# Optimization experiments

Hardware: AMD Instinct MI355X
Metric: run time of the kernel (lower is better)

The kernel has to match this reference:

```python
import jax, jax.numpy as jnp
import numpy as np

NEG_SLOPE = 0.2
EPS = 1e-6
K = 16


def vec_lna(x, Wf, Wd):
    # x: (B, Cin, 3, ...). Vector-neuron linear + VN-LeakyReLU.
    p = jnp.einsum('oc,bc...->bo...', Wf, x)          # features (B, Cout, 3, ...)
    d = jnp.einsum('oc,bc...->bo...', Wd, x)          # directions (B, Cd, 3, ...), Cd=Cout or 1 (shared)
    dot = jnp.sum(p * d, axis=2, keepdims=True)
    dsq = jnp.sum(d * d, axis=2, keepdims=True)
    p_ref = p - (dot / (dsq + EPS)) * d               # reflect negative part onto hyperplane
    return NEG_SLOPE * p + (1.0 - NEG_SLOPE) * jnp.where(dot >= 0, p, p_ref)


def knn_idx_fn(pts, k):
    # pts: (B, N, 3) -> (B, N, k) indices of k nearest neighbors (incl. self)
    sq = jnp.sum(pts * pts, axis=-1)                  # (B, N)
    d2 = sq[:, :, None] + sq[:, None, :] - 2.0 * jnp.einsum('bnd,bmd->bnm', pts, pts)
    _, idx = jax.lax.top_k(-d2, k)                    # smallest distances
    return idx


def graph_feature(x, idx):
    # x: (B, C, 3, N), idx: (B, N, k) -> (B, 2C, 3, N, k)
    nb = jax.vmap(lambda xb, ib: xb[:, :, ib])(x, idx)  # (B, C, 3, N, k)
    xc = x[..., None]
    return jnp.concatenate([nb - xc, jnp.broadcast_to(xc, nb.shape)], axis=1)


def _winit(key, co, ci):
    return jax.random.normal(key, (co, ci), dtype=jnp.float32) * np.sqrt(2.0 / ci).astype(np.float32)


def setup_inputs() -> dict:
    key = jax.random.key(0)
    ks = jax.random.split(key, 16)
    B, N = 4, 2048
    x = jax.random.normal(ks[0], (B, 3, N), dtype=jnp.float32)
    return {
        'x': x,
        'w1f': _winit(ks[1], 16, 2),   'w1d': _winit(ks[2], 16, 2),
        'w2f': _winit(ks[3], 32, 32),  'w2d': _winit(ks[4], 32, 32),
        'w3f': _winit(ks[5], 64, 64),  'w3d': _winit(ks[6], 64, 64),
        'w4f': _winit(ks[7], 128, 128),'w4d': _winit(ks[8], 128, 128),
        'wcf': _winit(ks[9], 128, 240),'wcd': _winit(ks[10], 1, 240),   # shared nonlinearity -> 1 dir channel
        'wi1f': _winit(ks[11], 128, 256), 'wi1d': _winit(ks[12], 128, 256),
        'wi2f': _winit(ks[13], 256, 128), 'wi2d': _winit(ks[14], 256, 128),
    }


def reference(x, w1f, w1d, w2f, w2d, w3f, w3d, w4f, w4d, wcf, wcd, wi1f, wi1d, wi2f, wi2d):
    # x: (B, 3, N)
    pts = jnp.transpose(x, (0, 2, 1))                 # (B, N, 3)
    idx = knn_idx_fn(pts, K)                          # (B, N, K) -- fixed graph (use_dg=False)
    h = x[:, None]                                    # (B, 1, 3, N)
    h = vec_lna(graph_feature(h, idx), w1f, w1d)
    x1 = h.mean(axis=-1)                              # (B, 16, 3, N)
    h = vec_lna(graph_feature(x1, idx), w2f, w2d)
    x2 = h.mean(axis=-1)                              # (B, 32, 3, N)
    h = vec_lna(graph_feature(x2, idx), w3f, w3d)
    x3 = h.mean(axis=-1)                              # (B, 64, 3, N)
    h = vec_lna(graph_feature(x3, idx), w4f, w4d)
    x4 = h.mean(axis=-1)                              # (B, 128, 3, N)
    xc = vec_lna(jnp.concatenate([x1, x2, x3, x4], axis=1), wcf, wcd)  # (B, 128, 3, N)
    xm = jnp.broadcast_to(xc.mean(axis=-1, keepdims=True), xc.shape)
    xcat = jnp.concatenate([xc, xm], axis=1)          # (B, 256, 3, N)
    x0 = vec_lna(vec_lna(xcat, wi1f, wi1d), wi2f, wi2d)
    inv = jnp.sum(xcat * x0, axis=2)                  # (B, 256, N) rotation-invariant features
    return inv
```

## Files before the change

kernel.cpp:

```cpp
#include <hip/hip_runtime.h>
#include <hip/hip_fp16.h>

#define NPTS  2048
#define BATCH 4
#define NBP   8192
#define MROWS 24576
#define KNN_K 16

typedef short bf16x8 __attribute__((ext_vector_type(8)));
typedef float f32x4  __attribute__((ext_vector_type(4)));

static __device__ __forceinline__ void split_bf16(float a, unsigned short& h, unsigned short& l)
{
    unsigned u = __float_as_uint(a);
    unsigned hr = (u + 0x7FFFu + ((u >> 16) & 1u)) & 0xFFFF0000u;
    h = (unsigned short)(hr >> 16);
    float rem = a - __uint_as_float(hr);
    unsigned v = __float_as_uint(rem);
    l = (unsigned short)((v + 0x7FFFu + ((v >> 16) & 1u)) >> 16);
}

static __device__ __forceinline__ float bf2(unsigned short h, unsigned short l)
{
    return __uint_as_float((unsigned)h << 16) + __uint_as_float((unsigned)l << 16);
}

static __device__ __forceinline__ float lna_scale(float dot, float dsq)
{
    return (dot < 0.f) ? 0.8f * dot * __builtin_amdgcn_rcpf(dsq + 1e-6f) : 0.f;
}

static __device__ __forceinline__ unsigned long long shfl_xor_u64(unsigned long long v, int mask)
{
    unsigned lo = (unsigned)v, hi = (unsigned)(v >> 32);
    lo = (unsigned)__shfl_xor((int)lo, mask, 64);
    hi = (unsigned)__shfl_xor((int)hi, mask, 64);
    return ((unsigned long long)hi << 32) | lo;
}

static __device__ __forceinline__ int xcd_swizzle(int i, int G)
{
    int batch  = (i >> 1) & 3;
    int within = ((i >> 3) << 1) | (i & 1);
    return batch * (G >> 2) + within;
}

static __device__ __forceinline__ float wbig_val(const float* __restrict__ Wf,
                                                 const float* __restrict__ Wd,
                                                 int j, int c, int O, int C)
{
    if (j < 2 * O) {
        int o = j >> 1;
        return (j & 1) ? Wd[o * 2 * C + c] : Wf[o * 2 * C + c];
    }
    int o = (j - 2 * O) >> 1;
    return (j & 1) ? (Wd[o * 2 * C + C + c] - Wd[o * 2 * C + c])
                   : (Wf[o * 2 * C + C + c] - Wf[o * 2 * C + c]);
}

static __device__ __forceinline__ int frag_ix(int r, int c, int RB)
{
    return (((c >> 5) * RB + (r >> 4)) * 64 + ((c >> 3) & 3) * 16 + (r & 15)) * 8 + (c & 7);
}

#define PC0 1572864
#define PC1 (PC0 + 4096)
#define PC2 (PC1 + 8192)
#define PC3 (PC2 + 32768)
#define PC4 (PC3 + 49152)
#define PC5 (PC4 + 32768)
#define PC6 (PC5 + 65536)
#define KNN_BLOCKS (NBP / 4)
#define PREP_BLOCKS (PC6 / 256)

__global__ __launch_bounds__(256) void prep_knn_kernel(
    const float* __restrict__ x, int* __restrict__ idx,
    __half* __restrict__ AH, float* __restrict__ AG,
    const float* __restrict__ w1f, const float* __restrict__ w1d,
    const float* __restrict__ w2f, const float* __restrict__ w2d,
    unsigned short* __restrict__ Wb2h, unsigned short* __restrict__ Wb2l,
    const float* __restrict__ w3f, const float* __restrict__ w3d,
    unsigned short* __restrict__ Wb3h, unsigned short* __restrict__ Wb3l,
    const float* __restrict__ w4f, const float* __restrict__ w4d,
    unsigned short* __restrict__ Wb4h, unsigned short* __restrict__ Wb4l,
    const float* __restrict__ wcf, const float* __restrict__ wcd,
    unsigned short* __restrict__ Wch, unsigned short* __restrict__ Wcl,
    const float* __restrict__ wi1f, const float* __restrict__ wi1d,
    unsigned short* __restrict__ Wi1h, unsigned short* __restrict__ Wi1l,
    const float* __restrict__ wi2f, const float* __restrict__ wi2d,
    unsigned short* __restrict__ Wi2h, unsigned short* __restrict__ Wi2l)
{
    __shared__ unsigned ksh[4][64 * 34];
    if (blockIdx.x < KNN_BLOCKS) {
        const int t  = threadIdx.x & 63;
        const int wq = threadIdx.x >> 6;
        const int bn = blockIdx.x * 4 + wq;
        const int b = bn >> 11;
        const int n = bn & (NPTS - 1);
        const float* xb = x + b * 3 * NPTS;
        const float qx = xb[n], qy = xb[NPTS + n], qz = xb[2 * NPTS + n];
        const float sqn = fmaf(qz, qz, fmaf(qy, qy, qx * qx));
        unsigned* ks = &ksh[wq][t * 34];

        unsigned gm[4];
        int ga[4];
#pragma unroll
        for (int g = 0; g < 4; g++) {
            unsigned kk[8];
#pragma unroll
            for (int j = 0; j < 8; j++) {
                const int i = g * 8 + j;
                const int m = (i << 6) + t;
                float mx = xb[m], my = xb[NPTS + m], mz = xb[2 * NPTS + m];
                float sqm = fmaf(mz, mz, fmaf(my, my, mx * mx));
                float dt  = fmaf(qz, mz, fmaf(qy, my, qx * mx));
                float d2  = sqn + sqm - 2.0f * dt;
                unsigned u = __float_as_uint(d2);
                u ^= (u & 0x80000000u) ? 0xFFFFFFFFu : 0x80000000u;
                kk[j] = u;
            }
            *(uint2*)&ks[g * 8 + 0] = make_uint2(kk[0], kk[1]);
            *(uint2*)&ks[g * 8 + 2] = make_uint2(kk[2], kk[3]);
            *(uint2*)&ks[g * 8 + 4] = make_uint2(kk[4], kk[5]);
            *(uint2*)&ks[g * 8 + 6] = make_uint2(kk[6], kk[7]);
            unsigned bg = kk[0];
            int ba = g * 8;
#pragma unroll
            for (int j = 1; j < 8; j++) {
                if (kk[j] < bg) { bg = kk[j]; ba = g * 8 + j; }
            }
            gm[g] = bg; ga[g] = ba;
        }
        unsigned lm = gm[0];
        int il = ga[0];
#pragma unroll
        for (int g = 1; g < 4; g++) if (gm[g] < lm) { lm = gm[g]; il = ga[g]; }

        unsigned long long pk = ((unsigned long long)lm << 32) | (unsigned)((il << 6) | t);
        int res = -1;
        for (int r = 0; r < KNN_K; r++) {
            unsigned long long w = pk;
#pragma unroll
            for (int off = 32; off > 0; off >>= 1) {
                unsigned long long o = shfl_xor_u64(w, off);
                w = (o < w) ? o : w;
            }
            if (t == r) res = (int)(w & 0xFFFFFFFFull);

            if (pk == w) {
                ks[il] = 0xFFFFFFFFu;
                const int g = il >> 3;
                unsigned bg = ks[g * 8];
                int ba = g * 8;
#pragma unroll
                for (int j = 1; j < 8; j++) {
                    unsigned kv = ks[g * 8 + j];
                    if (kv < bg) { bg = kv; ba = g * 8 + j; }
                }
                gm[g] = bg; ga[g] = ba;
                lm = gm[0]; il = ga[0];
#pragma unroll
                for (int g2 = 1; g2 < 4; g2++) if (gm[g2] < lm) { lm = gm[g2]; il = ga[g2]; }
                pk = ((unsigned long long)lm << 32) | (unsigned)((il << 6) | t);
            }
        }
        if (t < KNN_K) idx[bn * KNN_K + t] = res;
        return;
    }

    const int i = (blockIdx.x - KNN_BLOCKS) * 256 + threadIdx.x;
    if (i < PC0) {
        int o = i & 63;
        int row = i >> 6;
        int v = row % 3;
        int gp = row / 3;
        int b = gp >> 11;
        int n = gp & (NPTS - 1);
        float xv = x[(b * 3 + v) * NPTS + n];
        float wv = wbig_val(w1f, w1d, o, 0, 16, 1);
        float val = xv * wv;
        if (o < 32) AH[(size_t)row * 32 + o] = __float2half(val);
        else        AG[(size_t)row * 32 + o - 32] = val;
    } else if (i < PC6) {
        float v = 0.f;
        unsigned short *ph, *pl;
        int ix;
        if (i < PC1) {
            ix = i - PC0;
            int c = ix & 31, j = ix >> 5;
            if (c < 16) v = wbig_val(w2f, w2d, j, c, 32, 16);
            ph = Wb2h; pl = Wb2l;
        } else if (i < PC2) {
            ix = i - PC1;
            int c = ix & 31, j = ix >> 5;
            v = wbig_val(w3f, w3d, j, c, 64, 32);
            ph = Wb3h; pl = Wb3l;
        } else if (i < PC3) {
            ix = i - PC2;
            int c = ix & 63, r = ix >> 6;
            v = wbig_val(w4f, w4d, r, c, 128, 64);
            ph = Wb4h; pl = Wb4l;
            ix = frag_ix(r, c, 32);
        } else if (i < PC4) {
            ix = i - PC3;
            int c = ix & 255, r = ix >> 8;
            if (c < 240) {
                if (r < 128) v = wcf[r * 240 + c];
                else if (r < 129) v = wcd[(r - 128) * 240 + c];
            }
            ph = Wch; pl = Wcl;
            ix = frag_ix(r, c, 12);
        } else if (i < PC5) {
            ix = i - PC4;
            int c = ix & 127, r = ix >> 7;
            if (r < 128) v = wi1f[r * 256 + c];
            else v = wi1d[(r - 128) * 256 + c];
            ph = Wi1h; pl = Wi1l;
            ix = frag_ix(r, c, 16);
        } else {
            ix = i - PC5;
            int c = ix & 127, r = ix >> 7;
            int o = r >> 1;
            v = (r & 1) ? wi2d[o * 128 + c] : wi2f[o * 128 + c];
            ph = Wi2h; pl = Wi2l;
            ix = frag_ix(r, c, 32);
        }
        unsigned short h, l;
        split_bf16(v, h, l);
        ph[ix] = h; pl[ix] = l;
    }
}

template <int OIN, int NF>
__global__ __launch_bounds__(256, 3) void edge_gemm_kernel(
    const __half* __restrict__ AHin, const float* __restrict__ AGin,
    const int* __restrict__ idx,
    unsigned short* __restrict__ X240h, unsigned short* __restrict__ X240l, int ooff,
    const unsigned short* __restrict__ Wh, const unsigned short* __restrict__ Wl,
    __half* __restrict__ OUTA, float* __restrict__ OUTG)
{
    constexpr int PTS = 16;
    constexpr int NC = NF * 64;
    constexpr int twoO = NC / 2;
    constexpr int LDW = 40;
    constexpr int CPT = OIN / 16;
    constexpr int twoOin = 2 * OIN;

    __shared__ unsigned short Xsh[48][32];
    __shared__ unsigned short Xsl[48][32];
    __shared__ unsigned short wbh[NC][LDW];
    __shared__ unsigned short wbl[NC][LDW];
    __shared__ int sIdx[PTS][KNN_K];

    const int lb = xcd_swizzle(blockIdx.x, gridDim.x);
    const int tid = threadIdx.x;

    for (int rr = tid; rr < NC; rr += 256) {
#pragma unroll
        for (int scc = 0; scc < 4; scc++) {
            *(uint4*)&wbh[rr][scc * 8] = *(const uint4*)(Wh + (size_t)rr * 32 + scc * 8);
            *(uint4*)&wbl[rr][scc * 8] = *(const uint4*)(Wl + (size_t)rr * 32 + scc * 8);
        }
    }
    for (int j = tid; j < PTS * KNN_K; j += 256)
        sIdx[j >> 4][j & 15] = idx[(lb * PTS + (j >> 4)) * KNN_K + (j & 15)];
    __syncthreads();

    const int op = tid & 15;
    const int pt = tid >> 4;
    const int gp = lb * PTS + pt;
    const int b = gp >> 11;
    const int rown = gp * 3;
    const int bbase = (b << 11) * 3;

    float cg[3][2 * CPT];
#pragma unroll
    for (int v = 0; v < 3; v++) {
        if constexpr (CPT == 2) {
            float4 c4 = *(const float4*)&AGin[(size_t)(rown + v) * twoOin + 4 * op];
            cg[v][0] = c4.x; cg[v][1] = c4.y; cg[v][2] = c4.z; cg[v][3] = c4.w;
        } else {
            float2 c2 = *(const float2*)&AGin[(size_t)(rown + v) * twoOin + 2 * op];
            cg[v][0] = c2.x; cg[v][1] = c2.y;
        }
    }
    float am[CPT][3];
#pragma unroll
    for (int c0 = 0; c0 < CPT; c0++) { am[c0][0] = 0.f; am[c0][1] = 0.f; am[c0][2] = 0.f; }

#pragma unroll 2
    for (int k = 0; k < KNN_K; k++) {
        const int m = sIdx[pt][k];
        const __half* base = AHin + (size_t)(bbase + m * 3) * twoOin + 2 * CPT * op;
        float e[3][2 * CPT];
#pragma unroll
        for (int v = 0; v < 3; v++) {
            if constexpr (CPT == 2) {
                uint2 u = *(const uint2*)(base + (size_t)v * twoOin);
                float2 x0 = __half22float2(*(__half2*)&u.x);
                float2 x1 = __half22float2(*(__half2*)&u.y);
                e[v][0] = x0.x; e[v][1] = x0.y; e[v][2] = x1.x; e[v][3] = x1.y;
            } else {
                unsigned u = *(const unsigned*)(base + (size_t)v * twoOin);
                float2 x0 = __half22float2(*(__half2*)&u);
                e[v][0] = x0.x; e[v][1] = x0.y;
            }
        }
#pragma unroll
        for (int c0 = 0; c0 < CPT; c0++) {
            float p0 = e[0][2 * c0] + cg[0][2 * c0], d0 = e[0][2 * c0 + 1] + cg[0][2 * c0 + 1];
            float p1 = e[1][2 * c0] + cg[1][2 * c0], d1 = e[1][2 * c0 + 1] + cg[1][2 * c0 + 1];
            float p2 = e[2][2 * c0] + cg[2][2 * c0], d2 = e[2][2 * c0 + 1] + cg[2][2 * c0 + 1];
            float dot = fmaf(p2, d2, fmaf(p1, d1, p0 * d0));
            float dsq = fmaf(d2, d2, fmaf(d1, d1, d0 * d0));
            float s = lna_scale(dot, dsq);
            am[c0][0] += fmaf(-s, d0, p0);
            am[c0][1] += fmaf(-s, d1, p1);
            am[c0][2] += fmaf(-s, d2, p2);
        }
    }

#pragma unroll
    for (int v = 0; v < 3; v++) {
#pragma unroll
        for (int c0 = 0; c0 < CPT; c0++) {
            const int ch = CPT * op + c0;
            unsigned short h, l;
            split_bf16(am[c0][v] * 0.0625f, h, l);
            Xsh[pt * 3 + v][ch] = h;
            Xsl[pt * 3 + v][ch] = l;
            const size_t ob = (size_t)(rown + v) * 256 + ooff + ch;
            X240h[ob] = h; X240l[ob] = l;
        }
        if constexpr (CPT == 1) {
            Xsh[pt * 3 + v][16 + op] = 0;
            Xsl[pt * 3 + v][16 + op] = 0;
        }
    }
    __syncthreads();

    const int lane = tid & 63;
    const int wv = tid >> 6;
    const int mr = lane & 15;
    const int q  = lane >> 4;

    f32x4 acc[3][NF];
#pragma unroll
    for (int a = 0; a < 3; a++)
#pragma unroll
        for (int c = 0; c < NF; c++) acc[a][c] = (f32x4){0.f, 0.f, 0.f, 0.f};

    bf16x8 ah[3], al[3], bh[NF], bl[NF];
#pragma unroll
    for (int mf = 0; mf < 3; mf++) {
        ah[mf] = *(const bf16x8*)&Xsh[mf * 16 + mr][q * 8];
        al[mf] = *(const bf16x8*)&Xsl[mf * 16 + mr][q * 8];
    }
#pragma unroll
    for (int nf = 0; nf < NF; nf++) {
        const int wr = wv * 16 * NF + nf * 16 + mr;
        bh[nf] = *(const bf16x8*)&wbh[wr][q * 8];
        bl[nf] = *(const bf16x8*)&wbl[wr][q * 8];
    }
#pragma unroll
    for (int mf = 0; mf < 3; mf++)
#pragma unroll
        for (int nf = 0; nf < NF; nf++) {
            acc[mf][nf] = __builtin_amdgcn_mfma_f32_16x16x32_bf16(ah[mf], bh[nf], acc[mf][nf], 0, 0, 0);
            acc[mf][nf] = __builtin_amdgcn_mfma_f32_16x16x32_bf16(ah[mf], bl[nf], acc[mf][nf], 0, 0, 0);
            acc[mf][nf] = __builtin_amdgcn_mfma_f32_16x16x32_bf16(al[mf], bh[nf], acc[mf][nf], 0, 0, 0);
        }

    const int rbase = lb * 48;
#pragma unroll
    for (int nf = 0; nf < NF; nf++) {
        const int col = wv * 16 * NF + nf * 16 + mr;
#pragma unroll
        for (int mf = 0; mf < 3; mf++)
#pragma unroll
            for (int i = 0; i < 4; i++) {
                const int row = rbase + mf * 16 + q * 4 + i;
                const float val = acc[mf][nf][i];
                if (col < twoO) OUTA[(size_t)row * twoO + col] = __float2half(val);
                else            OUTG[(size_t)row * twoO + col - twoO] = val;
            }
    }
}

__global__ __launch_bounds__(256, 3) void edge_gemm4_kernel(
    const __half* __restrict__ AHin, const float* __restrict__ AGin,
    const int* __restrict__ idx,
    unsigned short* __restrict__ X240h, unsigned short* __restrict__ X240l,
    const unsigned short* __restrict__ Wh, const unsigned short* __restrict__ Wl,
    __half* __restrict__ OUTA, float* __restrict__ OUTG)
{
    __shared__ unsigned short Xsh[48][72];
    __shared__ unsigned short Xsl[48][72];
    __shared__ int sIdx[16][KNN_K];

    const int lb = xcd_swizzle(blockIdx.x, gridDim.x);
    const int tid = threadIdx.x;

    for (int j = tid; j < 16 * KNN_K; j += 256)
        sIdx[j >> 4][j & 15] = idx[(lb * 16 + (j >> 4)) * KNN_K + (j & 15)];
    __syncthreads();

    {
        const int op = tid & 15;
        const int pt = tid >> 4;
        const int gp = lb * 16 + pt;
        const int b = gp >> 11;
        const int rown = gp * 3;
        const int bbase = (b << 11) * 3;

        float cg[3][8];
#pragma unroll
        for (int v = 0; v < 3; v++) {
            const float* ag = &AGin[(size_t)(rown + v) * 128 + 8 * op];
            float4 c4a = *(const float4*)ag;
            float4 c4b = *(const float4*)(ag + 4);
            cg[v][0] = c4a.x; cg[v][1] = c4a.y; cg[v][2] = c4a.z; cg[v][3] = c4a.w;
            cg[v][4] = c4b.x; cg[v][5] = c4b.y; cg[v][6] = c4b.z; cg[v][7] = c4b.w;
        }
        float am[4][3];
#pragma unroll
        for (int c0 = 0; c0 < 4; c0++) { am[c0][0] = 0.f; am[c0][1] = 0.f; am[c0][2] = 0.f; }

        for (int k = 0; k < KNN_K; k++) {
            const int m = sIdx[pt][k];
            const __half* base = AHin + (size_t)(bbase + m * 3) * 128 + 8 * op;
            unsigned uw[3][4];
#pragma unroll
            for (int v = 0; v < 3; v++) {
                uint4 a = *(const uint4*)(base + (size_t)v * 128);
                uw[v][0] = a.x; uw[v][1] = a.y; uw[v][2] = a.z; uw[v][3] = a.w;
            }
#pragma unroll
            for (int c0 = 0; c0 < 4; c0++) {
                float2 e0 = __half22float2(*(__half2*)&uw[0][c0]);
                float2 e1 = __half22float2(*(__half2*)&uw[1][c0]);
                float2 e2 = __half22float2(*(__half2*)&uw[2][c0]);
                float p0 = e0.x + cg[0][2 * c0], d0 = e0.y + cg[0][2 * c0 + 1];
                float p1 = e1.x + cg[1][2 * c0], d1 = e1.y + cg[1][2 * c0 + 1];
                float p2 = e2.x + cg[2][2 * c0], d2 = e2.y + cg[2][2 * c0 + 1];
                float dot = fmaf(p2, d2, fmaf(p1, d1, p0 * d0));
                float dsq = fmaf(d2, d2, fmaf(d1, d1, d0 * d0));
                float s = lna_scale(dot, dsq);
                am[c0][0] += fmaf(-s, d0, p0);
                am[c0][1] += fmaf(-s, d1, p1);
                am[c0][2] += fmaf(-s, d2, p2);
            }
        }
#pragma unroll
        for (int v = 0; v < 3; v++)
#pragma unroll
            for (int c0 = 0; c0 < 4; c0++) {
                const int ch = 4 * op + c0;
                unsigned short h, l;
                split_bf16(am[c0][v] * 0.0625f, h, l);
                Xsh[pt * 3 + v][ch] = h;
                Xsl[pt * 3 + v][ch] = l;
                const size_t ob = (size_t)(rown + v) * 256 + 48 + ch;
                X240h[ob] = h; X240l[ob] = l;
            }
    }
    __syncthreads();

    const int lane = tid & 63;
    const int wv = tid >> 6;
    const int mr = lane & 15;
    const int q  = lane >> 4;

    f32x4 acc[3][8];
#pragma unroll
    for (int a = 0; a < 3; a++)
#pragma unroll
        for (int c = 0; c < 8; c++) acc[a][c] = (f32x4){0.f, 0.f, 0.f, 0.f};

    for (int ks = 0; ks < 2; ks++) {
        bf16x8 ah[3], al[3];
#pragma unroll
        for (int mf = 0; mf < 3; mf++) {
            ah[mf] = *(const bf16x8*)&Xsh[mf * 16 + mr][ks * 32 + q * 8];
            al[mf] = *(const bf16x8*)&Xsl[mf * 16 + mr][ks * 32 + q * 8];
        }
#pragma unroll
        for (int nf = 0; nf < 8; nf++) {
            const size_t wi = (size_t)((ks * 32 + wv * 8 + nf) * 64 + lane) * 8;
            const bf16x8 bh = *(const bf16x8*)(Wh + wi);
            const bf16x8 bl = *(const bf16x8*)(Wl + wi);
#pragma unroll
            for (int mf = 0; mf < 3; mf++) {
                acc[mf][nf] = __builtin_amdgcn_mfma_f32_16x16x32_bf16(ah[mf], bh, acc[mf][nf], 0, 0, 0);
                acc[mf][nf] = __builtin_amdgcn_mfma_f32_16x16x32_bf16(ah[mf], bl, acc[mf][nf], 0, 0, 0);
                acc[mf][nf] = __builtin_amdgcn_mfma_f32_16x16x32_bf16(al[mf], bh, acc[mf][nf], 0, 0, 0);
            }
        }
    }

    const int rbase = lb * 48;
#pragma unroll
    for (int nf = 0; nf < 8; nf++) {
        const int col = wv * 128 + nf * 16 + mr;
#pragma unroll
        for (int mf = 0; mf < 3; mf++)
#pragma unroll
            for (int i = 0; i < 4; i++) {
                const int row = rbase + mf * 16 + q * 4 + i;
                const float val = acc[mf][nf][i];
                if (col < 256) OUTA[(size_t)row * 256 + col] = __float2half(val);
                else           OUTG[(size_t)row * 256 + col - 256] = val;
            }
    }
}

#define EW_LDX 136
#define EW_LDT 133
__global__ __launch_bounds__(256, 4) void edge_wc_kernel(
    const __half* __restrict__ AHin, const float* __restrict__ AGin,
    const int* __restrict__ idx,
    const unsigned short* __restrict__ Xh, const unsigned short* __restrict__ Xl,
    const unsigned short* __restrict__ Wh, const unsigned short* __restrict__ Wl,
    unsigned short* __restrict__ oh, unsigned short* __restrict__ ol,
    float* __restrict__ part2)
{
    __shared__ __align__(16) char smem[48 * EW_LDX * 2 * 2];
    unsigned short (*x4h)[EW_LDX] = (unsigned short (*)[EW_LDX])smem;
    unsigned short (*x4l)[EW_LDX] = (unsigned short (*)[EW_LDX])(smem + 48 * EW_LDX * 2);
    float* tb = (float*)smem;
    __shared__ int sIdx[16][KNN_K];

    const int lb = xcd_swizzle(blockIdx.x, gridDim.x);
    const int tid = threadIdx.x;

    for (int j = tid; j < 16 * KNN_K; j += 256)
        sIdx[j >> 4][j & 15] = idx[(lb * 16 + (j >> 4)) * KNN_K + (j & 15)];
    __syncthreads();

    {
        const int op = tid & 15;
        const int pt = tid >> 4;
        const int gp = lb * 16 + pt;
        const int b = gp >> 11;
        const int rown = gp * 3;
        const int bbase = (b << 11) * 3;

        float cg[3][16];
#pragma unroll
        for (int v = 0; v < 3; v++) {
            const float* ag = &AGin[(size_t)(rown + v) * 256 + 16 * op];
#pragma unroll
            for (int t = 0; t < 4; t++) {
                float4 c4 = *(const float4*)(ag + 4 * t);
                cg[v][4 * t + 0] = c4.x; cg[v][4 * t + 1] = c4.y;
                cg[v][4 * t + 2] = c4.z; cg[v][4 * t + 3] = c4.w;
            }
        }
        float am[8][3];
#pragma unroll
        for (int c0 = 0; c0 < 8; c0++) { am[c0][0] = 0.f; am[c0][1] = 0.f; am[c0][2] = 0.f; }

        for (int k = 0; k < KNN_K; k++) {
            const int m = sIdx[pt][k];
            const __half* base = AHin + (size_t)(bbase + m * 3) * 256 + 16 * op;
            unsigned uw[3][8];
#pragma unroll
            for (int v = 0; v < 3; v++) {
                uint4 a  = *(const uint4*)(base + (size_t)v * 256);
                uint4 bq = *(const uint4*)(base + (size_t)v * 256 + 8);
                uw[v][0] = a.x;  uw[v][1] = a.y;  uw[v][2] = a.z;  uw[v][3] = a.w;
                uw[v][4] = bq.x; uw[v][5] = bq.y; uw[v][6] = bq.z; uw[v][7] = bq.w;
            }
#pragma unroll
            for (int c0 = 0; c0 < 8; c0++) {
                float2 e0 = __half22float2(*(__half2*)&uw[0][c0]);
                float2 e1 = __half22float2(*(__half2*)&uw[1][c0]);
                float2 e2 = __half22float2(*(__half2*)&uw[2][c0]);
                float p0 = e0.x + cg[0][2 * c0], d0 = e0.y + cg[0][2 * c0 + 1];
                float p1 = e1.x + cg[1][2 * c0], d1 = e1.y + cg[1][2 * c0 + 1];
                float p2 = e2.x + cg[2][2 * c0], d2 = e2.y + cg[2][2 * c0 + 1];
                float dot = fmaf(p2, d2, fmaf(p1, d1, p0 * d0));
                float dsq = fmaf(d2, d2, fmaf(d1, d1, d0 * d0));
                float s = lna_scale(dot, dsq);
                am[c0][0] += fmaf(-s, d0, p0);
                am[c0][1] += fmaf(-s, d1, p1);
                am[c0][2] += fmaf(-s, d2, p2);
            }
        }
#pragma unroll
        for (int v = 0; v < 3; v++)
#pragma unroll
            for (int c0 = 0; c0 < 8; c0++) {
                unsigned short h, l;
                split_bf16(am[c0][v] * 0.0625f, h, l);
                x4h[pt * 3 + v][8 * op + c0] = h;
                x4l[pt * 3 + v][8 * op + c0] = l;
            }
    }
    __syncthreads();

    const int lane = tid & 63;
    const int wv = tid >> 6;
    const int mr = lane & 15;
    const int q  = lane >> 4;
    const int rbase = lb * 48;

    f32x4 acc[3][3];
#pragma unroll
    for (int a = 0; a < 3; a++)
#pragma unroll
        for (int c = 0; c < 3; c++) acc[a][c] = (f32x4){0.f, 0.f, 0.f, 0.f};

    for (int k0 = 0; k0 < 256; k0 += 32) {
        const int kb = k0 + q * 8;
        bf16x8 ah[3], al[3], bh[3], bl[3];
#pragma unroll
        for (int mf = 0; mf < 3; mf++) {
            const int row = mf * 16 + mr;
            if (kb >= 112) {
                if (kb >= 240) {
                    ah[mf] = (bf16x8){0, 0, 0, 0, 0, 0, 0, 0};
                    al[mf] = (bf16x8){0, 0, 0, 0, 0, 0, 0, 0};
                } else {
                    ah[mf] = *(const bf16x8*)&x4h[row][kb - 112];
                    al[mf] = *(const bf16x8*)&x4l[row][kb - 112];
                }
            } else {
                const size_t xr = (size_t)(rbase + row) * 256 + kb;
                ah[mf] = *(const bf16x8*)(Xh + xr);
                al[mf] = *(const bf16x8*)(Xl + xr);
            }
        }
#pragma unroll
        for (int nf = 0; nf < 3; nf++) {
            const size_t wri = (size_t)((((k0 >> 5) * 12) + wv * 3 + nf) * 64 + lane) * 8;
            bh[nf] = *(const bf16x8*)(Wh + wri);
            bl[nf] = *(const bf16x8*)(Wl + wri);
        }
#pragma unroll
        for (int mf = 0; mf < 3; mf++)
#pragma unroll
            for (int nf = 0; nf < 3; nf++) {
                acc[mf][nf] = __builtin_amdgcn_mfma_f32_16x16x32_bf16(ah[mf], bh[nf], acc[mf][nf], 0, 0, 0);
                acc[mf][nf] = __builtin_amdgcn_mfma_f32_16x16x32_bf16(ah[mf], bl[nf], acc[mf][nf], 0, 0, 0);
                acc[mf][nf] = __builtin_amdgcn_mfma_f32_16x16x32_bf16(al[mf], bh[nf], acc[mf][nf], 0, 0, 0);
            }
    }
    __syncthreads();

#pragma unroll
    for (int mf = 0; mf < 3; mf++)
#pragma unroll
        for (int nf = 0; nf < 3; nf++) {
            const int col = wv * 48 + nf * 16 + mr;
            if (col <= 128) {
#pragma unroll
                for (int i = 0; i < 4; i++)
                    tb[(mf * 16 + q * 4 + i) * EW_LDT + col] = acc[mf][nf][i];
            }
        }
    __syncthreads();

    const int bp0 = lb * 16;
    float vacc[3] = {0.f, 0.f, 0.f};
#pragma unroll
    for (int it = 0; it < 8; it++) {
        const int item = it * 256 + tid;
        const int o = item & 127;
        const int pt = item >> 7;
        float p[3], d[3];
#pragma unroll
        for (int v = 0; v < 3; v++) {
            const int r = pt * 3 + v;
            p[v] = tb[r * EW_LDT + o];
            d[v] = tb[r * EW_LDT + 128];
        }
        float dot = fmaf(p[2], d[2], fmaf(p[1], d[1], p[0] * d[0]));
        float dsq = fmaf(d[2], d[2], fmaf(d[1], d[1], d[0] * d[0]));
        float s = lna_scale(dot, dsq);
#pragma unroll
        for (int v = 0; v < 3; v++) {
            float val = fmaf(-s, d[v], p[v]);
            vacc[v] += val;
            unsigned short h, l;
            split_bf16(val, h, l);
            const size_t ob = ((size_t)(bp0 + pt) * 3 + v) * 128 + o;
            oh[ob] = h; ol[ob] = l;
        }
    }

    __syncthreads();
    tb[tid] = vacc[0]; tb[256 + tid] = vacc[1]; tb[512 + tid] = vacc[2];
    __syncthreads();
    if (tid < 128) {
#pragma unroll
        for (int v = 0; v < 3; v++)
            part2[(size_t)lb * 384 + v * 128 + tid] =
                tb[v * 256 + tid] + tb[v * 256 + tid + 128];
    }
}

__global__ __launch_bounds__(128) void xm_reduce_ym_kernel(
    const float* __restrict__ part2,
    unsigned short* __restrict__ xmh, unsigned short* __restrict__ xml,
    const float* __restrict__ wi1f, const float* __restrict__ wi1d,
    float* __restrict__ ym)
{
    __shared__ float xs[128];
    const int bv = blockIdx.x;
    const int b = bv / 3;
    const int v = bv % 3;
    const int o = threadIdx.x;
    float acc = 0.f;
    for (int i = 0; i < 128; i++)
        acc += part2[(size_t)(b * 128 + i) * 384 + v * 128 + o];
    const float m = acc * (1.f / 2048.f);
    unsigned short h, l;
    split_bf16(m, h, l);
    xmh[bv * 128 + o] = h;
    xml[bv * 128 + o] = l;
    xs[o] = m;
    __syncthreads();
#pragma unroll
    for (int half = 0; half < 2; half++) {
        const int oo = half * 128 + o;
        const float* wrow = (oo < 128) ? (wi1f + (size_t)oo * 256 + 128)
                                       : (wi1d + (size_t)(oo - 128) * 256 + 128);
        float s = 0.f;
        for (int c = 0; c < 128; c++) s = fmaf(wrow[c], xs[c], s);
        ym[(size_t)bv * 256 + oo] = s;
    }
}

#define QI_LDY  136
#define QI_LDT  257
#define QI_LDT2 67
__global__ __launch_bounds__(256, 3) void gemm_ii_kernel(
    const unsigned short* __restrict__ xch, const unsigned short* __restrict__ xcl,
    const unsigned short* __restrict__ W1h, const unsigned short* __restrict__ W1l,
    const unsigned short* __restrict__ W2h, const unsigned short* __restrict__ W2l,
    const unsigned short* __restrict__ xmh, const unsigned short* __restrict__ xml,
    const float* __restrict__ ym,
    float* __restrict__ out)
{
    __shared__ __align__(16) char regA[25728];
    __shared__ __align__(16) unsigned short y1h[48][QI_LDY];
    __shared__ __align__(16) unsigned short y1l[48][QI_LDY];
    float* tb = (float*)regA;

    const int tid = threadIdx.x;
    const int lane = tid & 63;
    const int wv = tid >> 6;
    const int mr = lane & 15;
    const int q  = lane >> 4;
    const int lb = blockIdx.x;
    const int bm = lb * 48;
    const int bb = (lb * 16) >> 11;

    f32x4 acc[3][4];
#pragma unroll
    for (int a = 0; a < 3; a++)
#pragma unroll
        for (int c = 0; c < 4; c++) acc[a][c] = (f32x4){0.f, 0.f, 0.f, 0.f};

    for (int k0 = 0; k0 < 128; k0 += 32) {
        bf16x8 ah[3], al[3];
#pragma unroll
        for (int mf = 0; mf < 3; mf++) {
            const size_t xr = (size_t)(bm + mf * 16 + mr) * 128 + k0 + q * 8;
            ah[mf] = *(const bf16x8*)(xch + xr);
            al[mf] = *(const bf16x8*)(xcl + xr);
        }
        const int ks = k0 >> 5;
#pragma unroll
        for (int nf = 0; nf < 4; nf++) {
            const size_t wi = (size_t)((ks * 16 + wv * 4 + nf) * 64 + lane) * 8;
            const bf16x8 bh = *(const bf16x8*)(W1h + wi);
            const bf16x8 bl = *(const bf16x8*)(W1l + wi);
#pragma unroll
            for (int mf = 0; mf < 3; mf++) {
                acc[mf][nf] = __builtin_amdgcn_mfma_f32_16x16x32_bf16(ah[mf], bh, acc[mf][nf], 0, 0, 0);
                acc[mf][nf] = __builtin_amdgcn_mfma_f32_16x16x32_bf16(ah[mf], bl, acc[mf][nf], 0, 0, 0);
                acc[mf][nf] = __builtin_amdgcn_mfma_f32_16x16x32_bf16(al[mf], bh, acc[mf][nf], 0, 0, 0);
            }
        }
    }

    {
        const int oo = tid & 127;
        float ymp[3], ymd[3];
#pragma unroll
        for (int v = 0; v < 3; v++) {
            ymp[v] = ym[(size_t)(bb * 3 + v) * 256 + oo];
            ymd[v] = ym[(size_t)(bb * 3 + v) * 256 + 128 + oo];
        }
#pragma unroll
        for (int rh = 0; rh < 2; rh++) {
#pragma unroll
            for (int mf = 0; mf < 3; mf++)
#pragma unroll
                for (int nf = 0; nf < 4; nf++)
#pragma unroll
                    for (int i = 0; i < 4; i++) {
                        const int row = mf * 16 + q * 4 + i;
                        if (row >= rh * 24 && row < rh * 24 + 24)
                            tb[(size_t)(row - rh * 24) * QI_LDT + wv * 64 + nf * 16 + mr] = acc[mf][nf][i];
                    }
            __syncthreads();
#pragma unroll
            for (int it = 0; it < 4; it++) {
                const int item = it * 256 + tid;
                const int o = item & 127;
                const int ptl = item >> 7;
                const int pt = rh * 8 + ptl;
                float p[3], d[3];
#pragma unroll
                for (int v = 0; v < 3; v++) {
                    const int lr = 3 * ptl + v;
                    p[v] = tb[(size_t)lr * QI_LDT + o] + ymp[v];
                    d[v] = tb[(size_t)lr * QI_LDT + 128 + o] + ymd[v];
                }
                float dot = fmaf(p[2], d[2], fmaf(p[1], d[1], p[0] * d[0]));
                float dsq = fmaf(d[2], d[2], fmaf(d[1], d[1], d[0] * d[0]));
                float s = lna_scale(dot, dsq);
#pragma unroll
                for (int v = 0; v < 3; v++) {
                    unsigned short h, l;
                    split_bf16(fmaf(-s, d[v], p[v]), h, l);
                    y1h[pt * 3 + v][o] = h;
                    y1l[pt * 3 + v][o] = l;
                }
            }
            __syncthreads();
        }
    }

    f32x4 acc2[3][8];
#pragma unroll
    for (int a = 0; a < 3; a++)
#pragma unroll
        for (int c = 0; c < 8; c++) acc2[a][c] = (f32x4){0.f, 0.f, 0.f, 0.f};

    for (int k0 = 0; k0 < 128; k0 += 32) {
        bf16x8 ah[3], al[3];
#pragma unroll
        for (int mf = 0; mf < 3; mf++) {
            ah[mf] = *(const bf16x8*)&y1h[mf * 16 + mr][k0 + q * 8];
            al[mf] = *(const bf16x8*)&y1l[mf * 16 + mr][k0 + q * 8];
        }
#pragma unroll
        for (int nf = 0; nf < 8; nf++) {
            const size_t wi = (size_t)((((k0 >> 5) * 32) + wv * 8 + nf) * 64 + lane) * 8;
            const bf16x8 bh = *(const bf16x8*)(W2h + wi);
            const bf16x8 bl = *(const bf16x8*)(W2l + wi);
#pragma unroll
            for (int mf = 0; mf < 3; mf++) {
                acc2[mf][nf] = __builtin_amdgcn_mfma_f32_16x16x32_bf16(ah[mf], bh, acc2[mf][nf], 0, 0, 0);
                acc2[mf][nf] = __builtin_amdgcn_mfma_f32_16x16x32_bf16(ah[mf], bl, acc2[mf][nf], 0, 0, 0);
                acc2[mf][nf] = __builtin_amdgcn_mfma_f32_16x16x32_bf16(al[mf], bh, acc2[mf][nf], 0, 0, 0);
            }
        }
    }

    float* wt = tb + wv * (24 * QI_LDT2);
#pragma unroll
    for (int hf = 0; hf < 2; hf++) {
#pragma unroll
        for (int rh = 0; rh < 2; rh++) {
#pragma unroll
            for (int mf = 0; mf < 3; mf++)
#pragma unroll
                for (int nf2 = 0; nf2 < 4; nf2++)
#pragma unroll
                    for (int i = 0; i < 4; i++) {
                        const int row = mf * 16 + q * 4 + i;
                        if (row >= rh * 24 && row < rh * 24 + 24)
                            wt[(row - rh * 24) * QI_LDT2 + nf2 * 16 + mr] = acc2[mf][hf * 4 + nf2][i];
                    }
#pragma unroll
            for (int j = 0; j < 4; j++) {
                const int item = j * 64 + lane;
                const int ol = item & 31;
                const int ptl = item >> 5;
                const int pt = rh * 8 + ptl;
                const int og = wv * 64 + hf * 32 + ol;
                const int gp = lb * 16 + pt;
                float p[3], d[3], xc[3];
#pragma unroll
                for (int v = 0; v < 3; v++) {
                    const int lr = 3 * ptl + v;
                    p[v] = wt[lr * QI_LDT2 + 2 * ol];
                    d[v] = wt[lr * QI_LDT2 + 2 * ol + 1];
                    if (og < 128) {
                        const size_t ix = (size_t)(gp * 3 + v) * 128 + og;
                        xc[v] = bf2(xch[ix], xcl[ix]);
                    } else {
                        const size_t ix = (size_t)(bb * 3 + v) * 128 + og - 128;
                        xc[v] = bf2(xmh[ix], xml[ix]);
                    }
                }
                float dot = fmaf(p[2], d[2], fmaf(p[1], d[1], p[0] * d[0]));
                float dsq = fmaf(d[2], d[2], fmaf(d[1], d[1], d[0] * d[0]));
                float s = lna_scale(dot, dsq);
                float inv = 0.f;
#pragma unroll
                for (int v = 0; v < 3; v++)
                    inv = fmaf(xc[v], fmaf(-s, d[v], p[v]), inv);
                out[((size_t)bb * 256 + og) * NPTS + (gp & (NPTS - 1))] = inv;
            }
        }
    }
}

extern "C" void kernel_launch(void* const* d_in, const int* in_sizes, int n_in,
                              void* d_out, int out_size, void* d_ws, size_t ws_size,
                              hipStream_t stream)
{
    const float* x    = (const float*)d_in[0];
    const float* w1f  = (const float*)d_in[1];
    const float* w1d  = (const float*)d_in[2];
    const float* w2f  = (const float*)d_in[3];
    const float* w2d  = (const float*)d_in[4];
    const float* w3f  = (const float*)d_in[5];
    const float* w3d  = (const float*)d_in[6];
    const float* w4f  = (const float*)d_in[7];
    const float* w4d  = (const float*)d_in[8];
    const float* wcf  = (const float*)d_in[9];
    const float* wcd  = (const float*)d_in[10];
    const float* wi1f = (const float*)d_in[11];
    const float* wi1d = (const float*)d_in[12];
    const float* wi2f = (const float*)d_in[13];
    const float* wi2d = (const float*)d_in[14];
    float* out = (float*)d_out;

    float* F = (float*)d_ws;
    size_t off = 0;
    float* AG = F + off;                          off += (size_t)MROWS * 512;
    __half* AH = (__half*)(F + off);              off += (size_t)MROWS * 128;
    __half* AH2 = (__half*)(F + off);             off += (size_t)MROWS * 128;
    unsigned short* X240h = (unsigned short*)(F + off); off += (size_t)MROWS * 128;
    unsigned short* X240l = (unsigned short*)(F + off); off += (size_t)MROWS * 128;
    unsigned short* xc2h  = (unsigned short*)(F + off); off += (size_t)MROWS * 64;
    unsigned short* xc2l  = (unsigned short*)(F + off); off += (size_t)MROWS * 64;
    unsigned short* Wb2h = (unsigned short*)(F + off); off += 2048;
    unsigned short* Wb2l = (unsigned short*)(F + off); off += 2048;
    unsigned short* Wb3h = (unsigned short*)(F + off); off += 4096;
    unsigned short* Wb3l = (unsigned short*)(F + off); off += 4096;
    unsigned short* Wb4h = (unsigned short*)(F + off); off += 16384;
    unsigned short* Wb4l = (unsigned short*)(F + off); off += 16384;
    unsigned short* Wch  = (unsigned short*)(F + off); off += 24576;
    unsigned short* Wcl  = (unsigned short*)(F + off); off += 24576;
    unsigned short* Wi1h = (unsigned short*)(F + off); off += 32768;
    unsigned short* Wi1l = (unsigned short*)(F + off); off += 32768;
    unsigned short* Wi2h = (unsigned short*)(F + off); off += 32768;
    unsigned short* Wi2l = (unsigned short*)(F + off); off += 32768;
    float* part2 = F + off;                       off += (size_t)512 * 384;
    float* ym    = F + off;                       off += 12 * 256;
    unsigned short* xmph = (unsigned short*)(F + off); off += 768;
    unsigned short* xmpl = (unsigned short*)(F + off); off += 768;
    int* idx    = (int*)(F + off);                off += NBP * KNN_K;
    float* AG2 = AG + (size_t)MROWS * 256;

    prep_knn_kernel<<<KNN_BLOCKS + PREP_BLOCKS, 256, 0, stream>>>(
        x, idx, AH, AG, w1f, w1d,
        w2f, w2d, Wb2h, Wb2l, w3f, w3d, Wb3h, Wb3l, w4f, w4d, Wb4h, Wb4l,
        wcf, wcd, Wch, Wcl, wi1f, wi1d, Wi1h, Wi1l, wi2f, wi2d, Wi2h, Wi2l);

    edge_gemm_kernel<16, 2><<<NBP / 16, 256, 0, stream>>>(
        AH, AG, idx, X240h, X240l, 0, Wb2h, Wb2l, AH2, AG2);
    edge_gemm_kernel<32, 4><<<NBP / 16, 256, 0, stream>>>(
        AH2, AG2, idx, X240h, X240l, 16, Wb3h, Wb3l, AH, AG);
    edge_gemm4_kernel<<<NBP / 16, 256, 0, stream>>>(
        AH, AG, idx, X240h, X240l, Wb4h, Wb4l, AH2, AG2);

    edge_wc_kernel<<<NBP / 16, 256, 0, stream>>>(AH2, AG2, idx, X240h, X240l,
                                                 Wch, Wcl, xc2h, xc2l, part2);

    xm_reduce_ym_kernel<<<BATCH * 3, 128, 0, stream>>>(part2, xmph, xmpl, wi1f, wi1d, ym);

    gemm_ii_kernel<<<MROWS / 48, 256, 0, stream>>>(xc2h, xc2l, Wi1h, Wi1l,
                                                   Wi2h, Wi2l, xmph, xmpl, ym, out);

    (void)in_sizes; (void)n_in; (void)out_size; (void)ws_size;
}
```

Before: 251.6 us.

## Halve gemm_ii row tile to 24 rows and relax edge_gemm4 occupancy bound

gemm_ii_kernel now handles 8 points (24 rows) per block instead of 16, which doubles the grid and removes the two-pass row-half staging loops. The MMA fragments still cover 32 rows, so a third of the second fragment's work is padding that gets discarded, and the 24-row tile also reads 8 rows past it. The intent is more blocks, lower register and LDS pressure, and fewer barriers. Separately, edge_gemm4's launch bound drops from 3 to 2 blocks per CU, giving the compiler more registers at the cost of occupancy.

```diff
diff --git a/kernel.cpp b/kernel.cpp
--- a/kernel.cpp
+++ b/kernel.cpp
@@ -387,7 +387,7 @@
     }
 }
 
-__global__ __launch_bounds__(256, 3) void edge_gemm4_kernel(
+__global__ __launch_bounds__(256, 2) void edge_gemm4_kernel(
     const __half* __restrict__ AHin, const float* __restrict__ AGin,
     const int* __restrict__ idx,
     unsigned short* __restrict__ X240h, unsigned short* __restrict__ X240l,
@@ -744,8 +744,8 @@
     float* __restrict__ out)
 {
     __shared__ __align__(16) char regA[25728];
-    __shared__ __align__(16) unsigned short y1h[48][QI_LDY];
-    __shared__ __align__(16) unsigned short y1l[48][QI_LDY];
+    __shared__ __align__(16) unsigned short y1h[32][QI_LDY];
+    __shared__ __align__(16) unsigned short y1l[32][QI_LDY];
     float* tb = (float*)regA;
 
     const int tid = threadIdx.x;
@@ -754,19 +754,20 @@
     const int mr = lane & 15;
     const int q  = lane >> 4;
     const int lb = blockIdx.x;
-    const int bm = lb * 48;
-    const int bb = (lb * 16) >> 11;
-
-    f32x4 acc[3][4];
-#pragma unroll
-    for (int a = 0; a < 3; a++)
+    const int bm = lb * 24;
+    const int bp0 = lb * 8;
+    const int bb = bp0 >> 11;
+
+    f32x4 acc[2][4];
+#pragma unroll
+    for (int a = 0; a < 2; a++)
 #pragma unroll
         for (int c = 0; c < 4; c++) acc[a][c] = (f32x4){0.f, 0.f, 0.f, 0.f};
 
     for (int k0 = 0; k0 < 128; k0 += 32) {
-        bf16x8 ah[3], al[3];
-#pragma unroll
-        for (int mf = 0; mf < 3; mf++) {
+        bf16x8 ah[2], al[2];
+#pragma unroll
+        for (int mf = 0; mf < 2; mf++) {
             const size_t xr = (size_t)(bm + mf * 16 + mr) * 128 + k0 + q * 8;
             ah[mf] = *(const bf16x8*)(xch + xr);
             al[mf] = *(const bf16x8*)(xcl + xr);
@@ -778,7 +779,7 @@
             const bf16x8 bh = *(const bf16x8*)(W1h + wi);
             const bf16x8 bl = *(const bf16x8*)(W1l + wi);
 #pragma unroll
-            for (int mf = 0; mf < 3; mf++) {
+            for (int mf = 0; mf < 2; mf++) {
                 acc[mf][nf] = __builtin_amdgcn_mfma_f32_16x16x32_bf16(ah[mf], bh, acc[mf][nf], 0, 0, 0);
                 acc[mf][nf] = __builtin_amdgcn_mfma_f32_16x16x32_bf16(ah[mf], bl, acc[mf][nf], 0, 0, 0);
                 acc[mf][nf] = __builtin_amdgcn_mfma_f32_16x16x32_bf16(al[mf], bh, acc[mf][nf], 0, 0, 0);
@@ -786,6 +787,18 @@
         }
     }
 
+#pragma unroll
+    for (int mf = 0; mf < 2; mf++)
+#pragma unroll
+        for (int nf = 0; nf < 4; nf++)
+#pragma unroll
+            for (int i = 0; i < 4; i++) {
+                const int row = mf * 16 + q * 4 + i;
+                if (row < 24)
+                    tb[(size_t)row * QI_LDT + wv * 64 + nf * 16 + mr] = acc[mf][nf][i];
+            }
+    __syncthreads();
+
     {
         const int oo = tid & 127;
         float ymp[3], ymd[3];
@@ -795,56 +808,41 @@
             ymd[v] = ym[(size_t)(bb * 3 + v) * 256 + 128 + oo];
         }
 #pragma unroll
-        for (int rh = 0; rh < 2; rh++) {
-#pragma unroll
-            for (int mf = 0; mf < 3; mf++)
-#pragma unroll
-                for (int nf = 0; nf < 4; nf++)
-#pragma unroll
-                    for (int i = 0; i < 4; i++) {
-                        const int row = mf * 16 + q * 4 + i;
-                        if (row >= rh * 24 && row < rh * 24 + 24)
-                            tb[(size_t)(row - rh * 24) * QI_LDT + wv * 64 + nf * 16 + mr] = acc[mf][nf][i];
-                    }
-            __syncthreads();
-#pragma unroll
-            for (int it = 0; it < 4; it++) {
-                const int item = it * 256 + tid;
-                const int o = item & 127;
-                const int ptl = item >> 7;
-                const int pt = rh * 8 + ptl;
-                float p[3], d[3];
-#pragma unroll
-                for (int v = 0; v < 3; v++) {
-                    const int lr = 3 * ptl + v;
-                    p[v] = tb[(size_t)lr * QI_LDT + o] + ymp[v];
-                    d[v] = tb[(size_t)lr * QI_LDT + 128 + o] + ymd[v];
-                }
-                float dot = fmaf(p[2], d[2], fmaf(p[1], d[1], p[0] * d[0]));
-                float dsq = fmaf(d[2], d[2], fmaf(d[1], d[1], d[0] * d[0]));
-                float s = lna_scale(dot, dsq);
-#pragma unroll
-                for (int v = 0; v < 3; v++) {
-                    unsigned short h, l;
-                    split_bf16(fmaf(-s, d[v], p[v]), h, l);
-                    y1h[pt * 3 + v][o] = h;
-                    y1l[pt * 3 + v][o] = l;
-                }
-            }
-            __syncthreads();
-        }
-    }
-
-    f32x4 acc2[3][8];
-#pragma unroll
-    for (int a = 0; a < 3; a++)
+        for (int it = 0; it < 4; it++) {
+            const int item = it * 256 + tid;
+            const int o = item & 127;
+            const int pt = item >> 7;
+            float p[3], d[3];
+#pragma unroll
+            for (int v = 0; v < 3; v++) {
+                const int r = pt * 3 + v;
+                p[v] = tb[(size_t)r * QI_LDT + o] + ymp[v];
+                d[v] = tb[(size_t)r * QI_LDT + 128 + o] + ymd[v];
+            }
+            float dot = fmaf(p[2], d[2], fmaf(p[1], d[1], p[0] * d[0]));
+            float dsq = fmaf(d[2], d[2], fmaf(d[1], d[1], d[0] * d[0]));
+            float s = lna_scale(dot, dsq);
+#pragma unroll
+            for (int v = 0; v < 3; v++) {
+                unsigned short h, l;
+                split_bf16(fmaf(-s, d[v], p[v]), h, l);
+                y1h[pt * 3 + v][o] = h;
+                y1l[pt * 3 + v][o] = l;
+            }
+        }
+    }
+    __syncthreads();
+
+    f32x4 acc2[2][8];
+#pragma unroll
+    for (int a = 0; a < 2; a++)
 #pragma unroll
         for (int c = 0; c < 8; c++) acc2[a][c] = (f32x4){0.f, 0.f, 0.f, 0.f};
 
     for (int k0 = 0; k0 < 128; k0 += 32) {
-        bf16x8 ah[3], al[3];
-#pragma unroll
-        for (int mf = 0; mf < 3; mf++) {
+        bf16x8 ah[2], al[2];
+#pragma unroll
+        for (int mf = 0; mf < 2; mf++) {
             ah[mf] = *(const bf16x8*)&y1h[mf * 16 + mr][k0 + q * 8];
             al[mf] = *(const bf16x8*)&y1l[mf * 16 + mr][k0 + q * 8];
         }
@@ -854,7 +852,7 @@
             const bf16x8 bh = *(const bf16x8*)(W2h + wi);
             const bf16x8 bl = *(const bf16x8*)(W2l + wi);
 #pragma unroll
-            for (int mf = 0; mf < 3; mf++) {
+            for (int mf = 0; mf < 2; mf++) {
                 acc2[mf][nf] = __builtin_amdgcn_mfma_f32_16x16x32_bf16(ah[mf], bh, acc2[mf][nf], 0, 0, 0);
                 acc2[mf][nf] = __builtin_amdgcn_mfma_f32_16x16x32_bf16(ah[mf], bl, acc2[mf][nf], 0, 0, 0);
                 acc2[mf][nf] = __builtin_amdgcn_mfma_f32_16x16x32_bf16(al[mf], bh, acc2[mf][nf], 0, 0, 0);
@@ -866,48 +864,44 @@
 #pragma unroll
     for (int hf = 0; hf < 2; hf++) {
 #pragma unroll
-        for (int rh = 0; rh < 2; rh++) {
-#pragma unroll
-            for (int mf = 0; mf < 3; mf++)
-#pragma unroll
-                for (int nf2 = 0; nf2 < 4; nf2++)
-#pragma unroll
-                    for (int i = 0; i < 4; i++) {
-                        const int row = mf * 16 + q * 4 + i;
-                        if (row >= rh * 24 && row < rh * 24 + 24)
-                            wt[(row - rh * 24) * QI_LDT2 + nf2 * 16 + mr] = acc2[mf][hf * 4 + nf2][i];
-                    }
-#pragma unroll
-            for (int j = 0; j < 4; j++) {
-                const int item = j * 64 + lane;
-                const int ol = item & 31;
-                const int ptl = item >> 5;
-                const int pt = rh * 8 + ptl;
-                const int og = wv * 64 + hf * 32 + ol;
-                const int gp = lb * 16 + pt;
-                float p[3], d[3], xc[3];
-#pragma unroll
-                for (int v = 0; v < 3; v++) {
-                    const int lr = 3 * ptl + v;
-                    p[v] = wt[lr * QI_LDT2 + 2 * ol];
-                    d[v] = wt[lr * QI_LDT2 + 2 * ol + 1];
-                    if (og < 128) {
-                        const size_t ix = (size_t)(gp * 3 + v) * 128 + og;
-                        xc[v] = bf2(xch[ix], xcl[ix]);
-                    } else {
-                        const size_t ix = (size_t)(bb * 3 + v) * 128 + og - 128;
-                        xc[v] = bf2(xmh[ix], xml[ix]);
-                    }
+        for (int mf = 0; mf < 2; mf++)
+#pragma unroll
+            for (int nf2 = 0; nf2 < 4; nf2++)
+#pragma unroll
+                for (int i = 0; i < 4; i++) {
+                    const int row = mf * 16 + q * 4 + i;
+                    if (row < 24)
+                        wt[row * QI_LDT2 + nf2 * 16 + mr] = acc2[mf][hf * 4 + nf2][i];
                 }
-                float dot = fmaf(p[2], d[2], fmaf(p[1], d[1], p[0] * d[0]));
-                float dsq = fmaf(d[2], d[2], fmaf(d[1], d[1], d[0] * d[0]));
-                float s = lna_scale(dot, dsq);
-                float inv = 0.f;
-#pragma unroll
-                for (int v = 0; v < 3; v++)
-                    inv = fmaf(xc[v], fmaf(-s, d[v], p[v]), inv);
-                out[((size_t)bb * 256 + og) * NPTS + (gp & (NPTS - 1))] = inv;
-            }
+#pragma unroll
+        for (int j = 0; j < 4; j++) {
+            const int item = j * 64 + lane;
+            const int ol = item & 31;
+            const int pt = item >> 5;
+            const int og = wv * 64 + hf * 32 + ol;
+            const int gp = bp0 + pt;
+            float p[3], d[3], xc[3];
+#pragma unroll
+            for (int v = 0; v < 3; v++) {
+                const int lr = 3 * pt + v;
+                p[v] = wt[lr * QI_LDT2 + 2 * ol];
+                d[v] = wt[lr * QI_LDT2 + 2 * ol + 1];
+                if (og < 128) {
+                    const size_t ix = (size_t)(gp * 3 + v) * 128 + og;
+                    xc[v] = bf2(xch[ix], xcl[ix]);
+                } else {
+                    const size_t ix = (size_t)(bb * 3 + v) * 128 + og - 128;
+                    xc[v] = bf2(xmh[ix], xml[ix]);
+                }
+            }
+            float dot = fmaf(p[2], d[2], fmaf(p[1], d[1], p[0] * d[0]));
+            float dsq = fmaf(d[2], d[2], fmaf(d[1], d[1], d[0] * d[0]));
+            float s = lna_scale(dot, dsq);
+            float inv = 0.f;
+#pragma unroll
+            for (int v = 0; v < 3; v++)
+                inv = fmaf(xc[v], fmaf(-s, d[v], p[v]), inv);
+            out[((size_t)bb * 256 + og) * NPTS + (gp & (NPTS - 1))] = inv;
         }
     }
 }
@@ -978,7 +972,7 @@
 
     xm_reduce_ym_kernel<<<BATCH * 3, 128, 0, stream>>>(part2, xmph, xmpl, wi1f, wi1d, ym);
 
-    gemm_ii_kernel<<<MROWS / 48, 256, 0, stream>>>(xc2h, xc2l, Wi1h, Wi1l,
+    gemm_ii_kernel<<<MROWS / 24, 256, 0, stream>>>(xc2h, xc2l, Wi1h, Wi1l,
                                                    Wi2h, Wi2l, xmph, xmpl, ym, out);
 
     (void)in_sizes; (void)n_in; (void)out_size; (void)ws_size;
```

Result: slower. 257.5 us (+2.3%).
